# Kernel optimization log

Measured on AMD Instinct MI355X. Metric: run time of the kernel, lower is better.

Reference implementation:

```python
import jax, jax.numpy as jnp
import numpy as np

N_BINS = 10
THRESHOLD = 0.5
FOR_NEG_CLASS = False


def reference(outputs, labels):
    """Single-pass equivalent of CalibrationCurve.update starting from zeroed buffers.

    Returns jnp.stack([prob_sum, tp_sum, count]) of shape (3, N_BINS).
    Bin b covers (low[b], high[b]] with edges = linspace(-1e-6, 1, N_BINS+1),
    exactly matching the torch per-bin masked reductions, fused into one
    bucketize + three segment-sums (one HBM pass instead of 3*N_BINS).
    """
    if FOR_NEG_CLASS:
        outputs = 1.0 - outputs
        labels = 1.0 - labels
    edges = jnp.linspace(jnp.float32(-1e-6), jnp.float32(1.0), N_BINS + 1)
    high = edges[1:]   # upper bound per bin (inclusive)
    low0 = edges[0]    # global lower bound (exclusive)

    x = outputs.ravel()
    y = labels.ravel()
    # smallest b with x <= high[b]  (side='left': high[b-1] < x <= high[b])
    bin_idx = jnp.searchsorted(high, x, side='left')
    valid = (x > low0) & (x <= high[-1])
    # invalid elements get index N_BINS -> dropped by segment_sum (out of range)
    idx = jnp.where(valid, bin_idx, N_BINS)

    prob_sum = jax.ops.segment_sum(x, idx, num_segments=N_BINS)
    tp_sum = jax.ops.segment_sum((y > THRESHOLD).astype(jnp.float32), idx, num_segments=N_BINS)
    count = jax.ops.segment_sum(jnp.ones_like(x), idx, num_segments=N_BINS)
    return jnp.stack([prob_sum, tp_sum, count])  # (3, N_BINS)


def setup_inputs() -> dict:
    key = jax.random.key(0)
    k1, k2 = jax.random.split(key)
    outputs = jax.random.uniform(k1, (32, 1024, 1024), dtype=jnp.float32)
    labels = jax.random.uniform(k2, (32, 1024, 1024), dtype=jnp.float32)
    return {"outputs": outputs, "labels": labels}
```

## Files before the change

### kernel.cpp

```cpp
#include <hip/hip_runtime.h>

#define NBINS 10
#define PART_STRIDE 32

__global__ __launch_bounds__(256) void calib_hist(
    const float* __restrict__ outputs,
    const float* __restrict__ labels,
    float* __restrict__ partials,
    long n)
{
    const int tid = threadIdx.x;
    const float low0 = -1e-6f;
    const float step = (1.0f - low0) / 10.0f;

    float prob [NBINS];
    int   cnttp[NBINS];
#pragma unroll
    for (int b = 0; b < NBINS; ++b) { prob[b] = 0.0f; cnttp[b] = 0; }

    const long total4 = n >> 2;
    const float4* o4 = (const float4*)outputs;
    const float4* l4 = (const float4*)labels;
    const long gid = (long)blockIdx.x * blockDim.x + tid;
    const long gsz = (long)gridDim.x * blockDim.x;

    for (long i = gid; i < total4; i += gsz) {
        float4 o = o4[i];
        float4 l = l4[i];
        float xs[4] = {o.x, o.y, o.z, o.w};
        float ys[4] = {l.x, l.y, l.z, l.w};
#pragma unroll
        for (int k = 0; k < 4; ++k) {
            float x = xs[k];
            bool valid = (x > low0) & (x <= 1.0f);
            int e = (int)(x * 10.0f);
            e = e > 9 ? 9 : e;
            float fe  = (float)e;
            float hb0 = fmaf(fe,        step, low0);
            float hb1 = fmaf(fe + 1.0f, step, low0);
            int b = e + ((x > hb1) ? 1 : 0) - (((e > 0) & (x <= hb0)) ? 1 : 0);
            float px = valid ? x : 0.0f;
            int   pc = valid ? ((ys[k] > 0.5f) ? 0x10001 : 1) : 0;
#pragma unroll
            for (int bb = 0; bb < NBINS; ++bb) {
                bool m = (b == bb);
                prob [bb] += m ? px : 0.0f;
                cnttp[bb] += m ? pc : 0;
            }
        }
    }

    const long tail0 = total4 << 2;
    for (long j = tail0 + gid; j < n; j += gsz) {
        float x = outputs[j];
        float y = labels [j];
        bool valid = (x > low0) & (x <= 1.0f);
        int e = (int)(x * 10.0f);
        e = e > 9 ? 9 : e;
        float fe  = (float)e;
        float hb0 = fmaf(fe,        step, low0);
        float hb1 = fmaf(fe + 1.0f, step, low0);
        int b = e + ((x > hb1) ? 1 : 0) - (((e > 0) & (x <= hb0)) ? 1 : 0);
        float px = valid ? x : 0.0f;
        int   pc = valid ? ((y > 0.5f) ? 0x10001 : 1) : 0;
#pragma unroll
        for (int bb = 0; bb < NBINS; ++bb) {
            bool m = (b == bb);
            prob [bb] += m ? px : 0.0f;
            cnttp[bb] += m ? pc : 0;
        }
    }

#pragma unroll
    for (int bb = 0; bb < NBINS; ++bb) {
#pragma unroll
        for (int off = 1; off < 64; off <<= 1) {
            prob [bb] += __shfl_xor(prob [bb], off, 64);
            cnttp[bb] += __shfl_xor(cnttp[bb], off, 64);
        }
    }

    __shared__ float s_part[4][PART_STRIDE];
    const int w = tid >> 6;
    if ((tid & 63) == 0) {
#pragma unroll
        for (int bb = 0; bb < NBINS; ++bb) {
            int v = cnttp[bb];
            s_part[w][bb]           = prob[bb];
            s_part[w][NBINS + bb]   = (float)(v >> 16);
            s_part[w][2*NBINS + bb] = (float)(v & 0xFFFF);
        }
    }
    __syncthreads();
    if (tid < 3 * NBINS) {
        float s = s_part[0][tid] + s_part[1][tid] + s_part[2][tid] + s_part[3][tid];
        partials[(long)blockIdx.x * PART_STRIDE + tid] = s;
    }
}

__global__ __launch_bounds__(256) void calib_reduce(
    const float* __restrict__ partials, float* __restrict__ out, int nrows)
{
    const int s   = blockIdx.x;
    const int tid = threadIdx.x;
    double acc = 0.0;
    for (int r = tid; r < nrows; r += 256)
        acc += (double)partials[(long)r * PART_STRIDE + s];
#pragma unroll
    for (int off = 32; off > 0; off >>= 1)
        acc += __shfl_down(acc, off, 64);
    __shared__ double wsum[4];
    if ((tid & 63) == 0) wsum[tid >> 6] = acc;
    __syncthreads();
    if (tid == 0) out[s] = (float)(wsum[0] + wsum[1] + wsum[2] + wsum[3]);
}

extern "C" void kernel_launch(void* const* d_in, const int* in_sizes, int n_in,
                              void* d_out, int out_size, void* d_ws, size_t ws_size,
                              hipStream_t stream) {
    const float* outputs = (const float*)d_in[0];
    const float* labels  = (const float*)d_in[1];
    float* out = (float*)d_out;
    long n = (long)in_sizes[0];

    int nblocks = 2048;
    size_t need = (size_t)nblocks * PART_STRIDE * sizeof(float);
    if (ws_size < need) {
        nblocks = (int)(ws_size / (PART_STRIDE * sizeof(float)));
        if (nblocks < 1) nblocks = 1;
    }
    float* partials = (float*)d_ws;

    calib_hist  <<<nblocks, 256, 0, stream>>>(outputs, labels, partials, n);
    calib_reduce<<<3 * NBINS, 256, 0, stream>>>(partials, out, nblocks);
}
```

Baseline: 285.1 us.

## Replace per-thread register histogram with private LDS rows and 64-bit read-modify-write

Drops the per-element 10-way masked accumulation into registers. Each thread now keeps a private histogram row in shared memory (float prob sum packed with a 16+16-bit count/tp word) and updates its bin with a single 64-bit load/store. The end-of-block reduction becomes a strided LDS sum instead of wavefront shuffles, and the grid shrinks from 2048 to 1792 blocks. The change removes the ALU cost of the unrolled bin compare loop, but it adds LDS traffic on the critical path and lowers occupancy because of the roughly 22 KB of shared memory per block.

```diff
diff --git a/kernel.cpp b/kernel.cpp
--- a/kernel.cpp
+++ b/kernel.cpp
@@ -1,6 +1,7 @@
 #include <hip/hip_runtime.h>
 
 #define NBINS 10
+#define ROWW  22
 #define PART_STRIDE 32
 
 __global__ __launch_bounds__(256) void calib_hist(
@@ -9,14 +10,15 @@
     float* __restrict__ partials,
     long n)
 {
+    __shared__ __align__(16) unsigned int s_hist[256 * ROWW];
+
     const int tid = threadIdx.x;
+    for (int j = tid; j < 256 * ROWW; j += 256) s_hist[j] = 0u;
+    __syncthreads();
+
     const float low0 = -1e-6f;
     const float step = (1.0f - low0) / 10.0f;
-
-    float prob [NBINS];
-    int   cnttp[NBINS];
-#pragma unroll
-    for (int b = 0; b < NBINS; ++b) { prob[b] = 0.0f; cnttp[b] = 0; }
+    unsigned int* __restrict__ row = &s_hist[tid * ROWW];
 
     const long total4 = n >> 2;
     const float4* o4 = (const float4*)outputs;
@@ -34,19 +36,19 @@
             float x = xs[k];
             bool valid = (x > low0) & (x <= 1.0f);
             int e = (int)(x * 10.0f);
-            e = e > 9 ? 9 : e;
+            e = e < 0 ? 0 : (e > 9 ? 9 : e);
             float fe  = (float)e;
             float hb0 = fmaf(fe,        step, low0);
             float hb1 = fmaf(fe + 1.0f, step, low0);
             int b = e + ((x > hb1) ? 1 : 0) - (((e > 0) & (x <= hb0)) ? 1 : 0);
-            float px = valid ? x : 0.0f;
-            int   pc = valid ? ((ys[k] > 0.5f) ? 0x10001 : 1) : 0;
-#pragma unroll
-            for (int bb = 0; bb < NBINS; ++bb) {
-                bool m = (b == bb);
-                prob [bb] += m ? px : 0.0f;
-                cnttp[bb] += m ? pc : 0;
-            }
+            b = b < 0 ? 0 : (b > 9 ? 9 : b);
+            float        px = valid ? x : 0.0f;
+            unsigned int pc = valid ? ((ys[k] > 0.5f) ? 0x10001u : 1u) : 0u;
+            unsigned long long* p = (unsigned long long*)&row[2 * b];
+            unsigned long long v = *p;
+            float        pr = __uint_as_float((unsigned int)v) + px;
+            unsigned int ct = (unsigned int)(v >> 32) + pc;
+            *p = ((unsigned long long)ct << 32) | (unsigned long long)__float_as_uint(pr);
         }
     }
 
@@ -56,44 +58,46 @@
         float y = labels [j];
         bool valid = (x > low0) & (x <= 1.0f);
         int e = (int)(x * 10.0f);
-        e = e > 9 ? 9 : e;
+        e = e < 0 ? 0 : (e > 9 ? 9 : e);
         float fe  = (float)e;
         float hb0 = fmaf(fe,        step, low0);
         float hb1 = fmaf(fe + 1.0f, step, low0);
         int b = e + ((x > hb1) ? 1 : 0) - (((e > 0) & (x <= hb0)) ? 1 : 0);
-        float px = valid ? x : 0.0f;
-        int   pc = valid ? ((y > 0.5f) ? 0x10001 : 1) : 0;
-#pragma unroll
-        for (int bb = 0; bb < NBINS; ++bb) {
-            bool m = (b == bb);
-            prob [bb] += m ? px : 0.0f;
-            cnttp[bb] += m ? pc : 0;
-        }
+        b = b < 0 ? 0 : (b > 9 ? 9 : b);
+        float        px = valid ? x : 0.0f;
+        unsigned int pc = valid ? ((y > 0.5f) ? 0x10001u : 1u) : 0u;
+        unsigned long long* p = (unsigned long long*)&row[2 * b];
+        unsigned long long v = *p;
+        float        pr = __uint_as_float((unsigned int)v) + px;
+        unsigned int ct = (unsigned int)(v >> 32) + pc;
+        *p = ((unsigned long long)ct << 32) | (unsigned long long)__float_as_uint(pr);
     }
 
-#pragma unroll
-    for (int bb = 0; bb < NBINS; ++bb) {
-#pragma unroll
-        for (int off = 1; off < 64; off <<= 1) {
-            prob [bb] += __shfl_xor(prob [bb], off, 64);
-            cnttp[bb] += __shfl_xor(cnttp[bb], off, 64);
+    __syncthreads();
+
+    if (tid < 240) {
+        int slot  = tid % 30;
+        int chunk = tid / 30;
+        int b = slot % NBINS;
+        float acc = 0.0f;
+        int r0 = chunk * 32;
+        for (int r = r0; r < r0 + 32; ++r) {
+            unsigned int base = (unsigned int)r * ROWW + 2 * b;
+            if (slot < NBINS) {
+                acc += __uint_as_float(s_hist[base]);
+            } else {
+                unsigned int c = s_hist[base + 1];
+                acc += (slot < 2 * NBINS) ? (float)(c >> 16) : (float)(c & 0xFFFFu);
+            }
         }
-    }
-
-    __shared__ float s_part[4][PART_STRIDE];
-    const int w = tid >> 6;
-    if ((tid & 63) == 0) {
-#pragma unroll
-        for (int bb = 0; bb < NBINS; ++bb) {
-            int v = cnttp[bb];
-            s_part[w][bb]           = prob[bb];
-            s_part[w][NBINS + bb]   = (float)(v >> 16);
-            s_part[w][2*NBINS + bb] = (float)(v & 0xFFFF);
-        }
+        ((float*)s_hist)[(unsigned int)(chunk * 30 + slot) * ROWW + 20] = acc;
     }
     __syncthreads();
     if (tid < 3 * NBINS) {
-        float s = s_part[0][tid] + s_part[1][tid] + s_part[2][tid] + s_part[3][tid];
+        float s = 0.0f;
+#pragma unroll
+        for (int c = 0; c < 8; ++c)
+            s += ((float*)s_hist)[(unsigned int)(c * 30 + tid) * ROWW + 20];
         partials[(long)blockIdx.x * PART_STRIDE + tid] = s;
     }
 }
@@ -123,7 +127,7 @@
     float* out = (float*)d_out;
     long n = (long)in_sizes[0];
 
-    int nblocks = 2048;
+    int nblocks = 1792;
     size_t need = (size_t)nblocks * PART_STRIDE * sizeof(float);
     if (ws_size < need) {
         nblocks = (int)(ws_size / (PART_STRIDE * sizeof(float)));
```

Result: faster. 276.6 us (-3.0%).
